# Performance work log

Measured on AMD Instinct MI355X. Metric: run time of the kernel, lower is better.

The kernel has to match this reference:

```python
import jax, jax.numpy as jnp
import numpy as np

EPS = 1e-6

def _rmsnorm(x, gamma):
    rms = jax.lax.rsqrt(jnp.mean(x * x, axis=-1, keepdims=True) + EPS)
    return x * rms * gamma

def _rotate_half(x):
    d = x.shape[-1] // 2
    return jnp.concatenate((-x[..., d:], x[..., :d]), axis=-1)

def setup_inputs() -> dict:
    key = jax.random.key(0)
    ks = jax.random.split(key, 6)
    B, S, H, NH = 2, 4096, 1024, 16
    hd = H // NH
    hidden_states = jax.random.normal(ks[0], (B, S, H), dtype=jnp.float32)
    rope_cos = jax.random.uniform(ks[1], (1, S, hd), dtype=jnp.float32)
    rope_sin = jax.random.uniform(ks[2], (1, S, hd), dtype=jnp.float32)
    W_qkv = jax.random.normal(ks[3], (H, 3 * H), dtype=jnp.float32) * (H ** -0.5)
    W_o = jax.random.normal(ks[4], (H, H), dtype=jnp.float32) * (H ** -0.5)
    gamma_q = jnp.ones((hd,), dtype=jnp.float32)
    gamma_k = jnp.ones((hd,), dtype=jnp.float32)
    return {"hidden_states": hidden_states, "rope_cos": rope_cos, "rope_sin": rope_sin,
            "W_qkv": W_qkv, "W_o": W_o, "gamma_q": gamma_q, "gamma_k": gamma_k}

def reference(hidden_states, rope_cos, rope_sin, W_qkv, W_o, gamma_q, gamma_k):
    B, S, H = hidden_states.shape
    NH = 16
    hd = H // NH
    qkv = hidden_states @ W_qkv  # [B,S,3H]
    q, k, v = jnp.split(qkv, 3, axis=-1)
    def to_heads(x):
        return x.reshape(B, S, NH, hd).transpose(0, 2, 1, 3)  # [B,NH,S,hd]
    q, k, v = to_heads(q), to_heads(k), to_heads(v)
    q = _rmsnorm(q, gamma_q)
    k = _rmsnorm(k, gamma_k)
    cos = rope_cos[:, None, :, :]  # [1,1,S,hd]
    sin = rope_sin[:, None, :, :]
    q = q * cos + _rotate_half(q) * sin
    k = k * cos + _rotate_half(k) * sin
    scores = jnp.einsum('bhqd,bhkd->bhqk', q, k) / (hd ** 0.5)
    causal = jnp.tril(jnp.ones((S, S), dtype=bool))
    scores = jnp.where(causal, scores, -jnp.inf)
    attn = jax.nn.softmax(scores, axis=-1)
    out = jnp.einsum('bhqk,bhkd->bhqd', attn, v)
    out = out.transpose(0, 2, 1, 3).reshape(B, S, H)
    return out @ W_o
```

## Files before the change

### kernel.cpp

```cpp
#include <hip/hip_runtime.h>
#include <stdint.h>

typedef unsigned short u16;
typedef __attribute__((ext_vector_type(8))) u16   u16x8;
typedef __attribute__((ext_vector_type(4))) u16   u16x4;
typedef __attribute__((ext_vector_type(8))) __bf16 bf16x8;
typedef __attribute__((ext_vector_type(4))) float  f32x4;

__device__ __forceinline__ u16 f2bf(float f) {
  union { float f; unsigned u; } x; x.f = f;
  unsigned r = x.u + 0x7fffu + ((x.u >> 16) & 1u);
  return (u16)(r >> 16);
}
__device__ __forceinline__ float bf2f(u16 h) {
  union { unsigned u; float f; } x; x.u = ((unsigned)h) << 16;
  return x.f;
}
__device__ __forceinline__ float fexp2(float x) {
#if __has_builtin(__builtin_amdgcn_exp2f)
  return __builtin_amdgcn_exp2f(x);
#else
  return __expf(x * 0.69314718055994531f);
#endif
}
__device__ __forceinline__ void gload_lds16(const void* g, void* l) {
  __builtin_amdgcn_global_load_lds(
      (__attribute__((address_space(1))) void*)(void*)g,
      (__attribute__((address_space(3))) void*)l, 16, 0, 0);
}
__device__ __forceinline__ bf16x8 ldfrag(const u16* p) {
  return __builtin_bit_cast(bf16x8, *(const u16x8*)p);
}
#define MFMA_BF16(a, b, c) __builtin_amdgcn_mfma_f32_16x16x32_bf16(a, b, c, 0, 0, 0)

__global__ __launch_bounds__(256) void k_f32_to_bf16(const float* __restrict__ in,
                                                     u16* __restrict__ out, int n) {
  int i = (blockIdx.x * 256 + threadIdx.x) * 4;
  if (i >= n) return;
  float4 v = *(const float4*)(in + i);
  u16x4 o; o.x = f2bf(v.x); o.y = f2bf(v.y); o.z = f2bf(v.z); o.w = f2bf(v.w);
  *(u16x4*)(out + i) = o;
}

__global__ __launch_bounds__(256) void k_transpose_bf16(const float* __restrict__ in,
                                                        u16* __restrict__ out,
                                                        int R, int C) {
  __shared__ float tile[32][33];
  int c0 = blockIdx.x * 32, r0 = blockIdx.y * 32;
  int tx = threadIdx.x, ty = threadIdx.y;
#pragma unroll
  for (int i = 0; i < 32; i += 8)
    tile[ty + i][tx] = in[(size_t)(r0 + ty + i) * C + c0 + tx];
  __syncthreads();
#pragma unroll
  for (int i = 0; i < 32; i += 8)
    out[(size_t)(c0 + ty + i) * R + r0 + tx] = f2bf(tile[tx][ty + i]);
}

__global__ __launch_bounds__(256) void k_gemm_qkv(const u16* __restrict__ A,
                                                  const u16* __restrict__ Bt,
                                                  u16* __restrict__ Q,
                                                  u16* __restrict__ Kb,
                                                  u16* __restrict__ Vt) {
  const int K = 1024;
  __shared__ u16 As[128 * 32];
  __shared__ u16 Bs[128 * 32];
  int tid = threadIdx.x;
  int wave = tid >> 6, lane = tid & 63, quad = lane >> 4, l15 = lane & 15;
  int m0 = blockIdx.y * 128, n0 = blockIdx.x * 128;
  int wm = (wave >> 1) * 64, wn = (wave & 1) * 64;
  f32x4 acc[4][4] = {};
  const u16* Ag = A + (size_t)m0 * K;
  const u16* Bg = Bt + (size_t)n0 * K;
  int lr = lane >> 2, lk = (lane & 3) * 8;

  for (int k0 = 0; k0 < K; k0 += 32) {
    __syncthreads();
#pragma unroll
    for (int i = 0; i < 2; i++) {
      int c = wave * 2 + i;
      gload_lds16(Ag + (size_t)(c * 16 + lr) * K + k0 + lk, &As[c * 512]);
      gload_lds16(Bg + (size_t)(c * 16 + lr) * K + k0 + lk, &Bs[c * 512]);
    }
    __syncthreads();
    bf16x8 af[4], bf[4];
#pragma unroll
    for (int mi = 0; mi < 4; mi++) af[mi] = ldfrag(&As[(wm + mi * 16 + l15) * 32 + quad * 8]);
#pragma unroll
    for (int ni = 0; ni < 4; ni++) bf[ni] = ldfrag(&Bs[(wn + ni * 16 + l15) * 32 + quad * 8]);
#pragma unroll
    for (int mi = 0; mi < 4; mi++)
#pragma unroll
      for (int ni = 0; ni < 4; ni++)
        acc[mi][ni] = MFMA_BF16(af[mi], bf[ni], acc[mi][ni]);
  }
  int sec = n0 >> 10;
#pragma unroll
  for (int mi = 0; mi < 4; mi++) {
    int rowb = m0 + wm + mi * 16 + quad * 4;
#pragma unroll
    for (int ni = 0; ni < 4; ni++) {
      int col = n0 + wn + ni * 16 + l15;
      int cc = col & 1023, h = cc >> 6, d = cc & 63;
#pragma unroll
      for (int r = 0; r < 4; r++) {
        int rg = rowb + r, b = rg >> 12, s = rg & 4095;
        u16 v = f2bf(acc[mi][ni][r]);
        size_t bh = (size_t)(b * 16 + h);
        if (sec == 0)      Q [(bh * 4096 + s) * 64 + d] = v;
        else if (sec == 1) Kb[(bh * 4096 + s) * 64 + d] = v;
        else {
          int sp = (s & ~31) | (((s & 15) << 1) | ((s >> 4) & 1));
          Vt[(bh * 64 + d) * 4096 + sp] = v;
        }
      }
    }
  }
}

__global__ __launch_bounds__(256) void k_rms_rope(u16* __restrict__ buf,
                                                  const float* __restrict__ gamma,
                                                  const float* __restrict__ cosb,
                                                  const float* __restrict__ sinb,
                                                  float scale) {
  int rid = blockIdx.x * 16 + (threadIdx.x >> 4);
  int l = threadIdx.x & 15;
  int s = rid & 4095;
  int d0 = l * 4;
  size_t idx = (size_t)rid * 64 + d0;
  u16x4 xv = *(const u16x4*)(buf + idx);
  float x0 = bf2f(xv.x), x1 = bf2f(xv.y), x2 = bf2f(xv.z), x3 = bf2f(xv.w);
  float ss = x0 * x0 + x1 * x1 + x2 * x2 + x3 * x3;
#pragma unroll
  for (int off = 1; off < 16; off <<= 1) ss += __shfl_xor(ss, off);
  float rms = rsqrtf(ss * (1.0f / 64.0f) + 1e-6f);
  float4 g = *(const float4*)(gamma + d0);
  float n0 = x0 * rms * g.x, n1 = x1 * rms * g.y, n2 = x2 * rms * g.z, n3 = x3 * rms * g.w;
  float p0 = __shfl_xor(n0, 8), p1 = __shfl_xor(n1, 8);
  float p2 = __shfl_xor(n2, 8), p3 = __shfl_xor(n3, 8);
  float sgn = (l < 8) ? -1.f : 1.f;
  float4 c = *(const float4*)(cosb + s * 64 + d0);
  float4 sn = *(const float4*)(sinb + s * 64 + d0);
  u16x4 o;
  o.x = f2bf((n0 * c.x + sgn * p0 * sn.x) * scale);
  o.y = f2bf((n1 * c.y + sgn * p1 * sn.y) * scale);
  o.z = f2bf((n2 * c.z + sgn * p2 * sn.z) * scale);
  o.w = f2bf((n3 * c.w + sgn * p3 * sn.w) * scale);
  *(u16x4*)(buf + idx) = o;
}

__device__ __forceinline__ void stage_k(const u16* Kg0, int kj, u16* Kbuf,
                                        int wave, int klr, int klc) {
  const u16* Kg = Kg0 + (size_t)kj * 128 * 64;
#pragma unroll
  for (int i = 0; i < 4; i++) {
    int c = wave * 4 + i;
    gload_lds16(Kg + (size_t)(c * 8 + klr) * 64 + (klc ^ klr) * 8, Kbuf + c * 512);
  }
}
__device__ __forceinline__ void stage_v(const u16* Vg0, int kj, u16* Vbuf,
                                        int wave, int quad, int l15) {
  const u16* Vg = Vg0 + kj * 128;
#pragma unroll
  for (int i = 0; i < 4; i++) {
    int c = wave * 4 + i;
    int vr = c * 4 + quad;
    gload_lds16(Vg + (size_t)vr * 4096 + (l15 ^ (vr & 15)) * 8, Vbuf + c * 512);
  }
}

__global__ __launch_bounds__(256, 2) void k_attn(const u16* __restrict__ Qb,
                                                 const u16* __restrict__ Kg_all,
                                                 const u16* __restrict__ Vtb,
                                                 u16* __restrict__ Ob) {
  __shared__ u16 Ks[2][128 * 64];
  __shared__ u16 Vts[2][64 * 128];
  __shared__ u16 Ps[4][32 * 40];
  const int PSTR = 40;
  int t = blockIdx.x, bhi = blockIdx.y;
  int tid = threadIdx.x, wave = tid >> 6, lane = tid & 63, quad = lane >> 4, l15 = lane & 15;
  const u16* Kg0 = Kg_all + (size_t)bhi * 4096 * 64;
  const u16* Vg0 = Vtb + (size_t)bhi * 64 * 4096;
  u16* Pw = Ps[wave];
  int klr = lane >> 3, klc = lane & 7;
  int b = bhi >> 4, h = bhi & 15;

  u16x8 ou;
#pragma unroll
  for (int i = 0; i < 8; i++) ou[i] = 0x3F80;
  bf16x8 ones = __builtin_bit_cast(bf16x8, ou);
  const f32x4 minit = {-47.f, -47.f, -47.f, -47.f};

#pragma unroll 1
  for (int tt = 0; tt < 2; tt++) {
    int qi = (tt == 0) ? (31 - t) : t;
    const u16* Qg = Qb + ((size_t)bhi * 4096 + qi * 128) * 64;
    bf16x8 aq[2][2];
#pragma unroll
    for (int mi = 0; mi < 2; mi++)
#pragma unroll
      for (int ks = 0; ks < 2; ks++)
        aq[mi][ks] = ldfrag(Qg + (size_t)(wave * 32 + mi * 16 + l15) * 64 + ks * 32 + quad * 8);
    f32x4 oacc[2][4] = {};
    f32x4 lacc[2] = {};

    if (tt) __builtin_amdgcn_s_barrier();
    stage_k(Kg0, 0, Ks[0], wave, klr, klc);
    stage_v(Vg0, 0, Vts[0], wave, quad, l15);

#pragma unroll 1
    for (int kj = 0; kj <= qi; kj++) {
      int cur = kj & 1;
      asm volatile("s_waitcnt vmcnt(0)" ::: "memory");
      __builtin_amdgcn_s_barrier();
      if (kj < qi) {
        stage_k(Kg0, kj + 1, Ks[cur ^ 1], wave, klr, klc);
        stage_v(Vg0, kj + 1, Vts[cur ^ 1], wave, quad, l15);
      }
      f32x4 sa[2][8];
#pragma unroll
      for (int mi = 0; mi < 2; mi++)
#pragma unroll
        for (int nb = 0; nb < 8; nb++) sa[mi][nb] = minit;
      __builtin_amdgcn_s_setprio(1);
#pragma unroll
      for (int ks = 0; ks < 2; ks++) {
#pragma unroll
        for (int nb = 0; nb < 8; nb++) {
          bf16x8 bk = ldfrag(&Ks[cur][(nb * 16 + l15) * 64 + (((ks * 4 + quad) ^ (l15 & 7)) << 3)]);
          sa[0][nb] = MFMA_BF16(aq[0][ks], bk, sa[0][nb]);
          sa[1][nb] = MFMA_BF16(aq[1][ks], bk, sa[1][nb]);
        }
      }
      __builtin_amdgcn_s_setprio(0);
      if (kj == qi) {
#pragma unroll
        for (int mi = 0; mi < 2; mi++)
#pragma unroll
          for (int nb = 0; nb < 8; nb++)
#pragma unroll
            for (int r = 0; r < 4; r++) {
              int rowi = wave * 32 + mi * 16 + quad * 4 + r;
              int coli = nb * 16 + l15;
              if (coli > rowi) sa[mi][nb][r] = -1e30f;
            }
      }
#pragma unroll
      for (int mi = 0; mi < 2; mi++)
#pragma unroll
        for (int nb = 0; nb < 8; nb++)
#pragma unroll
          for (int r = 0; r < 4; r++)
            sa[mi][nb][r] = fexp2(sa[mi][nb][r]);
#pragma unroll
      for (int ks = 0; ks < 4; ks++) {
        bf16x8 ap[2];
#pragma unroll
        for (int mi = 0; mi < 2; mi++) {
#pragma unroll
          for (int r = 0; r < 4; r++) {
            int prow = mi * 16 + quad * 4 + r;
            float lo = sa[mi][2 * ks][r], hi = sa[mi][2 * ks + 1][r];
            uint32_t pk;
            asm("v_cvt_pk_bf16_f32 %0, %1, %2" : "=v"(pk) : "v"(lo), "v"(hi));
            *(uint32_t*)&Pw[prow * PSTR + 2 * l15] = pk;
          }
          ap[mi] = ldfrag(&Pw[(mi * 16 + l15) * PSTR + quad * 8]);
        }
        __builtin_amdgcn_s_setprio(1);
#pragma unroll
        for (int oni = 0; oni < 4; oni++) {
          bf16x8 bv = ldfrag(&Vts[cur][(oni * 16 + l15) * 128 + (((ks * 4 + quad) ^ l15) << 3)]);
          oacc[0][oni] = MFMA_BF16(ap[0], bv, oacc[0][oni]);
          oacc[1][oni] = MFMA_BF16(ap[1], bv, oacc[1][oni]);
        }
        lacc[0] = MFMA_BF16(ap[0], ones, lacc[0]);
        lacc[1] = MFMA_BF16(ap[1], ones, lacc[1]);
        __builtin_amdgcn_s_setprio(0);
      }
    }
#pragma unroll
    for (int mi = 0; mi < 2; mi++)
#pragma unroll
      for (int oni = 0; oni < 4; oni++)
#pragma unroll
        for (int r = 0; r < 4; r++) {
          float v = oacc[mi][oni][r] / lacc[mi][r];
          int srow = qi * 128 + wave * 32 + mi * 16 + quad * 4 + r;
          int d = oni * 16 + l15;
          Ob[((size_t)(b * 4096 + srow)) * 1024 + h * 64 + d] = f2bf(v);
        }
  }
}

__global__ __launch_bounds__(256) void k_gemm_out(const u16* __restrict__ A,
                                                  const u16* __restrict__ Bt,
                                                  float* __restrict__ C) {
  const int K = 1024, N = 1024;
  __shared__ u16 As[128 * 32];
  __shared__ u16 Bs[128 * 32];
  int tid = threadIdx.x;
  int wave = tid >> 6, lane = tid & 63, quad = lane >> 4, l15 = lane & 15;
  int m0 = blockIdx.y * 128, n0 = blockIdx.x * 128;
  int wm = (wave >> 1) * 64, wn = (wave & 1) * 64;
  f32x4 acc[4][4] = {};
  const u16* Ag = A + (size_t)m0 * K;
  const u16* Bg = Bt + (size_t)n0 * K;
  int lr = lane >> 2, lk = (lane & 3) * 8;

  for (int k0 = 0; k0 < K; k0 += 32) {
    __syncthreads();
#pragma unroll
    for (int i = 0; i < 2; i++) {
      int c = wave * 2 + i;
      gload_lds16(Ag + (size_t)(c * 16 + lr) * K + k0 + lk, &As[c * 512]);
      gload_lds16(Bg + (size_t)(c * 16 + lr) * K + k0 + lk, &Bs[c * 512]);
    }
    __syncthreads();
    bf16x8 af[4], bf[4];
#pragma unroll
    for (int mi = 0; mi < 4; mi++) af[mi] = ldfrag(&As[(wm + mi * 16 + l15) * 32 + quad * 8]);
#pragma unroll
    for (int ni = 0; ni < 4; ni++) bf[ni] = ldfrag(&Bs[(wn + ni * 16 + l15) * 32 + quad * 8]);
#pragma unroll
    for (int mi = 0; mi < 4; mi++)
#pragma unroll
      for (int ni = 0; ni < 4; ni++)
        acc[mi][ni] = MFMA_BF16(af[mi], bf[ni], acc[mi][ni]);
  }
#pragma unroll
  for (int mi = 0; mi < 4; mi++) {
    int rowb = m0 + wm + mi * 16 + quad * 4;
#pragma unroll
    for (int ni = 0; ni < 4; ni++) {
      int col = n0 + wn + ni * 16 + l15;
#pragma unroll
      for (int r = 0; r < 4; r++)
        C[(size_t)(rowb + r) * N + col] = acc[mi][ni][r];
    }
  }
}

extern "C" void kernel_launch(void* const* d_in, const int* in_sizes, int n_in,
                              void* d_out, int out_size, void* d_ws, size_t ws_size,
                              hipStream_t stream) {
  (void)in_sizes; (void)n_in; (void)out_size; (void)ws_size;
  const float* hs   = (const float*)d_in[0];
  const float* cosb = (const float*)d_in[1];
  const float* sinb = (const float*)d_in[2];
  const float* wqkv = (const float*)d_in[3];
  const float* wo   = (const float*)d_in[4];
  const float* gq   = (const float*)d_in[5];
  const float* gk   = (const float*)d_in[6];
  float* out = (float*)d_out;

  char* ws = (char*)d_ws;
  u16* Xb    = (u16*)(ws);
  u16* Wqkvt = (u16*)(ws + 16777216);
  u16* Wot   = (u16*)(ws + 23068672);
  u16* Qb    = (u16*)(ws + 25165824);
  u16* Kb    = (u16*)(ws + 41943040);
  u16* Vtb   = (u16*)(ws + 58720256);
  u16* Ab    = (u16*)(ws + 75497472);

  k_f32_to_bf16<<<8192, 256, 0, stream>>>(hs, Xb, 8388608);
  k_transpose_bf16<<<dim3(96, 32), dim3(32, 8), 0, stream>>>(wqkv, Wqkvt, 1024, 3072);
  k_transpose_bf16<<<dim3(32, 32), dim3(32, 8), 0, stream>>>(wo, Wot, 1024, 1024);
  k_gemm_qkv<<<dim3(24, 64), 256, 0, stream>>>(Xb, Wqkvt, Qb, Kb, Vtb);
  k_rms_rope<<<8192, 256, 0, stream>>>(Qb, gq, cosb, sinb, 0.18033688011112042f);
  k_rms_rope<<<8192, 256, 0, stream>>>(Kb, gk, cosb, sinb, 1.0f);
  k_attn<<<dim3(16, 32), 256, 0, stream>>>(Qb, Kb, Vtb, Ab);
  k_gemm_out<<<dim3(8, 64), 256, 0, stream>>>(Ab, Wot, out);
}
```

Before: 346.7 us.

## Double-buffer LDS tiles in QKV and output GEMMs to overlap loads

Both projection GEMMs now keep two LDS buffers for the A and B tiles. The next k-slice is prefetched with direct global-to-LDS loads while the current slice is consumed by MFMA, and the loop uses one barrier per iteration instead of two. This aims to hide global memory latency behind compute. It doubles LDS use per block, which may reduce occupancy, and it relies on the single barrier plus vmcnt wait to keep the buffer reuse safe.

```diff
diff --git a/kernel.cpp b/kernel.cpp
--- a/kernel.cpp
+++ b/kernel.cpp
@@ -63,8 +63,8 @@
                                                   u16* __restrict__ Kb,
                                                   u16* __restrict__ Vt) {
   const int K = 1024;
-  __shared__ u16 As[128 * 32];
-  __shared__ u16 Bs[128 * 32];
+  __shared__ u16 As[2][128 * 32];
+  __shared__ u16 Bs[2][128 * 32];
   int tid = threadIdx.x;
   int wave = tid >> 6, lane = tid & 63, quad = lane >> 4, l15 = lane & 15;
   int m0 = blockIdx.y * 128, n0 = blockIdx.x * 128;
@@ -74,20 +74,29 @@
   const u16* Bg = Bt + (size_t)n0 * K;
   int lr = lane >> 2, lk = (lane & 3) * 8;
 
+#pragma unroll
+  for (int i = 0; i < 2; i++) {
+    int c = wave * 2 + i;
+    gload_lds16(Ag + (size_t)(c * 16 + lr) * K + lk, &As[0][c * 512]);
+    gload_lds16(Bg + (size_t)(c * 16 + lr) * K + lk, &Bs[0][c * 512]);
+  }
   for (int k0 = 0; k0 < K; k0 += 32) {
-    __syncthreads();
-#pragma unroll
-    for (int i = 0; i < 2; i++) {
-      int c = wave * 2 + i;
-      gload_lds16(Ag + (size_t)(c * 16 + lr) * K + k0 + lk, &As[c * 512]);
-      gload_lds16(Bg + (size_t)(c * 16 + lr) * K + k0 + lk, &Bs[c * 512]);
-    }
-    __syncthreads();
+    int cur = (k0 >> 5) & 1;
+    asm volatile("s_waitcnt vmcnt(0)" ::: "memory");
+    __builtin_amdgcn_s_barrier();
+    if (k0 + 32 < K) {
+#pragma unroll
+      for (int i = 0; i < 2; i++) {
+        int c = wave * 2 + i;
+        gload_lds16(Ag + (size_t)(c * 16 + lr) * K + k0 + 32 + lk, &As[cur ^ 1][c * 512]);
+        gload_lds16(Bg + (size_t)(c * 16 + lr) * K + k0 + 32 + lk, &Bs[cur ^ 1][c * 512]);
+      }
+    }
     bf16x8 af[4], bf[4];
 #pragma unroll
-    for (int mi = 0; mi < 4; mi++) af[mi] = ldfrag(&As[(wm + mi * 16 + l15) * 32 + quad * 8]);
-#pragma unroll
-    for (int ni = 0; ni < 4; ni++) bf[ni] = ldfrag(&Bs[(wn + ni * 16 + l15) * 32 + quad * 8]);
+    for (int mi = 0; mi < 4; mi++) af[mi] = ldfrag(&As[cur][(wm + mi * 16 + l15) * 32 + quad * 8]);
+#pragma unroll
+    for (int ni = 0; ni < 4; ni++) bf[ni] = ldfrag(&Bs[cur][(wn + ni * 16 + l15) * 32 + quad * 8]);
 #pragma unroll
     for (int mi = 0; mi < 4; mi++)
 #pragma unroll
@@ -297,8 +306,8 @@
                                                   const u16* __restrict__ Bt,
                                                   float* __restrict__ C) {
   const int K = 1024, N = 1024;
-  __shared__ u16 As[128 * 32];
-  __shared__ u16 Bs[128 * 32];
+  __shared__ u16 As[2][128 * 32];
+  __shared__ u16 Bs[2][128 * 32];
   int tid = threadIdx.x;
   int wave = tid >> 6, lane = tid & 63, quad = lane >> 4, l15 = lane & 15;
   int m0 = blockIdx.y * 128, n0 = blockIdx.x * 128;
@@ -308,20 +317,29 @@
   const u16* Bg = Bt + (size_t)n0 * K;
   int lr = lane >> 2, lk = (lane & 3) * 8;
 
+#pragma unroll
+  for (int i = 0; i < 2; i++) {
+    int c = wave * 2 + i;
+    gload_lds16(Ag + (size_t)(c * 16 + lr) * K + lk, &As[0][c * 512]);
+    gload_lds16(Bg + (size_t)(c * 16 + lr) * K + lk, &Bs[0][c * 512]);
+  }
   for (int k0 = 0; k0 < K; k0 += 32) {
-    __syncthreads();
-#pragma unroll
-    for (int i = 0; i < 2; i++) {
-      int c = wave * 2 + i;
-      gload_lds16(Ag + (size_t)(c * 16 + lr) * K + k0 + lk, &As[c * 512]);
-      gload_lds16(Bg + (size_t)(c * 16 + lr) * K + k0 + lk, &Bs[c * 512]);
-    }
-    __syncthreads();
+    int cur = (k0 >> 5) & 1;
+    asm volatile("s_waitcnt vmcnt(0)" ::: "memory");
+    __builtin_amdgcn_s_barrier();
+    if (k0 + 32 < K) {
+#pragma unroll
+      for (int i = 0; i < 2; i++) {
+        int c = wave * 2 + i;
+        gload_lds16(Ag + (size_t)(c * 16 + lr) * K + k0 + 32 + lk, &As[cur ^ 1][c * 512]);
+        gload_lds16(Bg + (size_t)(c * 16 + lr) * K + k0 + 32 + lk, &Bs[cur ^ 1][c * 512]);
+      }
+    }
     bf16x8 af[4], bf[4];
 #pragma unroll
-    for (int mi = 0; mi < 4; mi++) af[mi] = ldfrag(&As[(wm + mi * 16 + l15) * 32 + quad * 8]);
-#pragma unroll
-    for (int ni = 0; ni < 4; ni++) bf[ni] = ldfrag(&Bs[(wn + ni * 16 + l15) * 32 + quad * 8]);
+    for (int mi = 0; mi < 4; mi++) af[mi] = ldfrag(&As[cur][(wm + mi * 16 + l15) * 32 + quad * 8]);
+#pragma unroll
+    for (int ni = 0; ni < 4; ni++) bf[ni] = ldfrag(&Bs[cur][(wn + ni * 16 + l15) * 32 + quad * 8]);
 #pragma unroll
     for (int mi = 0; mi < 4; mi++)
 #pragma unroll
```

After: 357.3 us. 1.03x slower.

## Double K-tile depth to 64 with XOR-swizzled LDS layout in projection GEMMs

Applied to the files above, without the earlier changes.

Both the QKV and output projection GEMMs now stage 64-wide K slices per iteration instead of 32, halving the number of barrier pairs and loop iterations. The LDS tiles use an XOR swizzle on 16-byte chunks, applied to the global load address and the fragment reads, so that row-strided fragment loads avoid bank conflicts. This doubles LDS use per block, which may reduce occupancy, and there is still no double buffering.

```diff
diff --git a/kernel.cpp b/kernel.cpp
--- a/kernel.cpp
+++ b/kernel.cpp
@@ -63,8 +63,8 @@
                                                   u16* __restrict__ Kb,
                                                   u16* __restrict__ Vt) {
   const int K = 1024;
-  __shared__ u16 As[128 * 32];
-  __shared__ u16 Bs[128 * 32];
+  __shared__ u16 As[128 * 64];
+  __shared__ u16 Bs[128 * 64];
   int tid = threadIdx.x;
   int wave = tid >> 6, lane = tid & 63, quad = lane >> 4, l15 = lane & 15;
   int m0 = blockIdx.y * 128, n0 = blockIdx.x * 128;
@@ -72,27 +72,32 @@
   f32x4 acc[4][4] = {};
   const u16* Ag = A + (size_t)m0 * K;
   const u16* Bg = Bt + (size_t)n0 * K;
-  int lr = lane >> 2, lk = (lane & 3) * 8;
-
-  for (int k0 = 0; k0 < K; k0 += 32) {
+  int klr = lane >> 3, klc = lane & 7;
+
+  for (int k0 = 0; k0 < K; k0 += 64) {
+    if (k0) __syncthreads();
+#pragma unroll
+    for (int i = 0; i < 4; i++) {
+      int c = wave * 4 + i;
+      gload_lds16(Ag + (size_t)(c * 8 + klr) * K + k0 + (klc ^ klr) * 8, &As[c * 512]);
+      gload_lds16(Bg + (size_t)(c * 8 + klr) * K + k0 + (klc ^ klr) * 8, &Bs[c * 512]);
+    }
     __syncthreads();
 #pragma unroll
-    for (int i = 0; i < 2; i++) {
-      int c = wave * 2 + i;
-      gload_lds16(Ag + (size_t)(c * 16 + lr) * K + k0 + lk, &As[c * 512]);
-      gload_lds16(Bg + (size_t)(c * 16 + lr) * K + k0 + lk, &Bs[c * 512]);
-    }
-    __syncthreads();
-    bf16x8 af[4], bf[4];
-#pragma unroll
-    for (int mi = 0; mi < 4; mi++) af[mi] = ldfrag(&As[(wm + mi * 16 + l15) * 32 + quad * 8]);
-#pragma unroll
-    for (int ni = 0; ni < 4; ni++) bf[ni] = ldfrag(&Bs[(wn + ni * 16 + l15) * 32 + quad * 8]);
-#pragma unroll
-    for (int mi = 0; mi < 4; mi++)
+    for (int ks = 0; ks < 2; ks++) {
+      bf16x8 af[4], bf[4];
+#pragma unroll
+      for (int mi = 0; mi < 4; mi++)
+        af[mi] = ldfrag(&As[(wm + mi * 16 + l15) * 64 + (((ks * 4 + quad) ^ (l15 & 7)) << 3)]);
 #pragma unroll
       for (int ni = 0; ni < 4; ni++)
-        acc[mi][ni] = MFMA_BF16(af[mi], bf[ni], acc[mi][ni]);
+        bf[ni] = ldfrag(&Bs[(wn + ni * 16 + l15) * 64 + (((ks * 4 + quad) ^ (l15 & 7)) << 3)]);
+#pragma unroll
+      for (int mi = 0; mi < 4; mi++)
+#pragma unroll
+        for (int ni = 0; ni < 4; ni++)
+          acc[mi][ni] = MFMA_BF16(af[mi], bf[ni], acc[mi][ni]);
+    }
   }
   int sec = n0 >> 10;
 #pragma unroll
@@ -297,8 +302,8 @@
                                                   const u16* __restrict__ Bt,
                                                   float* __restrict__ C) {
   const int K = 1024, N = 1024;
-  __shared__ u16 As[128 * 32];
-  __shared__ u16 Bs[128 * 32];
+  __shared__ u16 As[128 * 64];
+  __shared__ u16 Bs[128 * 64];
   int tid = threadIdx.x;
   int wave = tid >> 6, lane = tid & 63, quad = lane >> 4, l15 = lane & 15;
   int m0 = blockIdx.y * 128, n0 = blockIdx.x * 128;
@@ -306,27 +311,32 @@
   f32x4 acc[4][4] = {};
   const u16* Ag = A + (size_t)m0 * K;
   const u16* Bg = Bt + (size_t)n0 * K;
-  int lr = lane >> 2, lk = (lane & 3) * 8;
-
-  for (int k0 = 0; k0 < K; k0 += 32) {
+  int klr = lane >> 3, klc = lane & 7;
+
+  for (int k0 = 0; k0 < K; k0 += 64) {
+    if (k0) __syncthreads();
+#pragma unroll
+    for (int i = 0; i < 4; i++) {
+      int c = wave * 4 + i;
+      gload_lds16(Ag + (size_t)(c * 8 + klr) * K + k0 + (klc ^ klr) * 8, &As[c * 512]);
+      gload_lds16(Bg + (size_t)(c * 8 + klr) * K + k0 + (klc ^ klr) * 8, &Bs[c * 512]);
+    }
     __syncthreads();
 #pragma unroll
-    for (int i = 0; i < 2; i++) {
-      int c = wave * 2 + i;
-      gload_lds16(Ag + (size_t)(c * 16 + lr) * K + k0 + lk, &As[c * 512]);
-      gload_lds16(Bg + (size_t)(c * 16 + lr) * K + k0 + lk, &Bs[c * 512]);
-    }
-    __syncthreads();
-    bf16x8 af[4], bf[4];
-#pragma unroll
-    for (int mi = 0; mi < 4; mi++) af[mi] = ldfrag(&As[(wm + mi * 16 + l15) * 32 + quad * 8]);
-#pragma unroll
-    for (int ni = 0; ni < 4; ni++) bf[ni] = ldfrag(&Bs[(wn + ni * 16 + l15) * 32 + quad * 8]);
-#pragma unroll
-    for (int mi = 0; mi < 4; mi++)
+    for (int ks = 0; ks < 2; ks++) {
+      bf16x8 af[4], bf[4];
+#pragma unroll
+      for (int mi = 0; mi < 4; mi++)
+        af[mi] = ldfrag(&As[(wm + mi * 16 + l15) * 64 + (((ks * 4 + quad) ^ (l15 & 7)) << 3)]);
 #pragma unroll
       for (int ni = 0; ni < 4; ni++)
-        acc[mi][ni] = MFMA_BF16(af[mi], bf[ni], acc[mi][ni]);
+        bf[ni] = ldfrag(&Bs[(wn + ni * 16 + l15) * 64 + (((ks * 4 + quad) ^ (l15 & 7)) << 3)]);
+#pragma unroll
+      for (int mi = 0; mi < 4; mi++)
+#pragma unroll
+        for (int ni = 0; ni < 4; ni++)
+          acc[mi][ni] = MFMA_BF16(af[mi], bf[ni], acc[mi][ni]);
+    }
   }
 #pragma unroll
   for (int mi = 0; mi < 4; mi++) {
```

Result: faster. 328.6 us (-5.2%).
